# Performance work log

Measured on AMD Instinct MI355X. Metric: run time of the kernel, lower is better.

The kernel has to match this reference:

```python
import jax, jax.numpy as jnp
import numpy as np

NDIM = 3
IMG_SIZE = (192, 192, 192)
CPS = (5, 5, 5)
CP_GRID = (42, 42, 42)


def bspline_kernel_1d(stride):
    # cubic B-spline sampled at (i - radius)/stride, length 4*stride-1
    n = 4 * stride - 1
    t = np.abs((np.arange(n) - n // 2) / float(stride))
    vals = np.where(t < 1.0, 2.0 / 3.0 + (0.5 * t - 1.0) * t ** 2,
                    np.where(t < 2.0, -((t - 2.0) ** 3) / 6.0, 0.0))
    return jnp.asarray(vals, dtype=jnp.float32)


def conv_transpose1d_lastaxis(x, kernel, stride, padding):
    # depthwise transposed conv along last axis; same kernel for every channel,
    # so fold all leading dims into the batch and use a single-channel conv
    # with lhs_dilation (equivalent to conv_transpose; kernel is symmetric).
    shp = x.shape
    K = kernel.shape[0]
    x2 = x.reshape(-1, 1, shp[-1])  # [N, C=1, L]
    w = kernel.reshape(1, 1, K)     # [O, I, W]
    pad = K - 1 - padding
    y = jax.lax.conv_general_dilated(
        x2, w, window_strides=(1,), padding=[(pad, pad)],
        lhs_dilation=(stride,), dimension_numbers=("NCW", "OIW", "NCW"))
    return y.reshape(shp[:-1] + (y.shape[-1],))


def setup_inputs() -> dict:
    key = jax.random.key(0)
    v = jax.random.normal(key, (4, NDIM) + CP_GRID, dtype=jnp.float32)
    return {"v": v}


def reference(v) -> jnp.ndarray:
    kernels = [bspline_kernel_1d(s) for s in CPS]
    for i in range(NDIM):
        k = kernels[i]
        s = CPS[i]
        p = (k.shape[0] - 1) // 2
        x = jnp.moveaxis(v, i + 2, -1)
        x = conv_transpose1d_lastaxis(x, k, s, p)
        v = jnp.moveaxis(x, -1, i + 2)
    # crop: slice(s, s + img_size) per spatial dim
    slicer = (slice(None), slice(None)) + tuple(
        slice(CPS[i], CPS[i] + IMG_SIZE[i]) for i in range(NDIM))
    return v[slicer]
```

## Files before the change

### kernel.cpp

```cpp
#include <hip/hip_runtime.h>


#define CPN 42
#define IMG 192
#define TXX 6
#define TYY 6
#define NTHREADS 256
#define SLICE (CPN * CPN * CPN)

__device__ __forceinline__ float bsp_w_rt(int r, int d) {
  double f = (double)r / 5.0;
  double g = (double)(5 - r) / 5.0;
  double w;
  if (d == 0)      { w = g * g * g / 6.0; }
  else if (d == 1) { w = 2.0 / 3.0 + (0.5 * f - 1.0) * f * f; }
  else if (d == 2) { w = 2.0 / 3.0 + (0.5 * g - 1.0) * g * g; }
  else             { w = f * f * f / 6.0; }
  return (float)w;
}

__global__ void __launch_bounds__(NTHREADS) ffd_kernel(
    const float* __restrict__ v, float* __restrict__ out) {
  const int tid = threadIdx.x;
  const int w = tid >> 6;
  const int lane = tid & 63;
  const int bx = blockIdx.x;
  const int by = blockIdx.y;
  const int sl = blockIdx.z;
  const int x0 = bx * TXX;
  const int y0 = by * TYY;

  __shared__ float wtab[20];
  if (tid < 20) wtab[tid] = bsp_w_rt(tid >> 2, tid & 3);
  __syncthreads();

  const int q = lane < 48 ? lane : 47;
  const int c0 = (4 * q) / 5;
  float wz[4][5];
#pragma unroll
  for (int k = 0; k < 4; ++k) {
    int z = 4 * q + k;
    int c = z / 5;
    int r = z - 5 * c;
    int off = c - c0;
#pragma unroll
    for (int t = 0; t < 5; ++t) {
      int d = t - off;
      wz[k][t] = (d >= 0 && d < 4) ? wtab[r * 4 + d] : 0.0f;
    }
  }

  const float* vs = v + (size_t)sl * SLICE;
  float* os = out + (size_t)sl * ((size_t)IMG * IMG * IMG);
  const int cc = lane < 42 ? lane : 41;

  for (int i = 0; i < 9; ++i) {
    int col = w + 4 * i;
    int xi = col / 6;
    int yi = col - 6 * xi;
    int x = x0 + xi;
    int y = y0 + yi;
    int ax = x / 5, rx = x - 5 * ax;
    int ay = y / 5, ry = y - 5 * ay;
    float wx0 = wtab[rx * 4 + 0], wx1 = wtab[rx * 4 + 1];
    float wx2 = wtab[rx * 4 + 2], wx3 = wtab[rx * 4 + 3];
    float wy0 = wtab[ry * 4 + 0], wy1 = wtab[ry * 4 + 1];
    float wy2 = wtab[ry * 4 + 2], wy3 = wtab[ry * 4 + 3];

    const float* vb = vs + (ax * CPN + ay) * CPN + cc;
    float t2 = 0.0f;
#pragma unroll
    for (int dx = 0; dx < 4; ++dx) {
      const float* vp = vb + dx * (CPN * CPN);
      float s = wy0 * vp[0];
      s = fmaf(wy1, vp[CPN], s);
      s = fmaf(wy2, vp[2 * CPN], s);
      s = fmaf(wy3, vp[3 * CPN], s);
      float wx = (dx == 0) ? wx0 : (dx == 1) ? wx1 : (dx == 2) ? wx2 : wx3;
      t2 = fmaf(wx, s, t2);
    }

    int t2i = __float_as_int(t2);
    float s[5];
#pragma unroll
    for (int t = 0; t < 5; ++t)
      s[t] = __int_as_float(
          __builtin_amdgcn_ds_bpermute((c0 + t) << 2, t2i));

    float res[4];
#pragma unroll
    for (int k = 0; k < 4; ++k) {
      float a = wz[k][0] * s[0];
      a = fmaf(wz[k][1], s[1], a);
      a = fmaf(wz[k][2], s[2], a);
      a = fmaf(wz[k][3], s[3], a);
      a = fmaf(wz[k][4], s[4], a);
      res[k] = a;
    }

    if (lane < 48) {
      float4 val = make_float4(res[0], res[1], res[2], res[3]);
      *reinterpret_cast<float4*>(
          os + (size_t)(x * IMG + y) * IMG + 4 * lane) = val;
    }
  }
}

extern "C" void kernel_launch(void* const* d_in, const int* in_sizes, int n_in,
                              void* d_out, int out_size, void* d_ws, size_t ws_size,
                              hipStream_t stream) {
  (void)in_sizes; (void)n_in; (void)d_ws; (void)ws_size; (void)out_size;
  const float* v = (const float*)d_in[0];
  float* out = (float*)d_out;
  dim3 grid(IMG / TXX, IMG / TYY, 12);
  ffd_kernel<<<grid, NTHREADS, 0, stream>>>(v, out);
}
```

Before: 386.0 us.

## Restructure B-spline upsampling into per-x-plane separable passes through shared memory

Each block now handles one output x-plane of one slice. It first collapses the x-direction into a control-point plane in LDS, then expands along y into a second LDS buffer, and finally applies the z weights and writes full rows. This removes the redundant 16-point global gathers per output column and the cross-lane permutes. The block index is also swizzled across slices. The cost is extra LDS use and barriers, with some idle lanes in the z pass.

Result: faster. 349.8 us (-9.4%).

```diff
diff --git a/kernel.cpp b/kernel.cpp
--- a/kernel.cpp
+++ b/kernel.cpp
@@ -3,10 +3,12 @@
 
 #define CPN 42
 #define IMG 192
-#define TXX 6
-#define TYY 6
 #define NTHREADS 256
 #define SLICE (CPN * CPN * CPN)
+#define PLANE (CPN * CPN)
+#define NBLK (12 * IMG)
+
+typedef float v4f __attribute__((ext_vector_type(4)));
 
 __device__ __forceinline__ float bsp_w_rt(int r, int d) {
   double f = (double)r / 5.0;
@@ -22,20 +24,28 @@
 __global__ void __launch_bounds__(NTHREADS) ffd_kernel(
     const float* __restrict__ v, float* __restrict__ out) {
   const int tid = threadIdx.x;
-  const int w = tid >> 6;
+  const int bid = blockIdx.x;
+  const int n  = (bid & 7) * (NBLK / 8) + (bid >> 3);
+  const int sl = n / IMG;
+  const int x  = n - sl * IMG;
+  const int ax = x / 5;
+  const int rx = x - 5 * ax;
+
+  __shared__ v4f  wq[5];
+  __shared__ float t1[PLANE];
+  __shared__ float t2[IMG * CPN];
+
+  if (tid < 5) {
+    v4f qv;
+    qv.x = bsp_w_rt(tid, 0); qv.y = bsp_w_rt(tid, 1);
+    qv.z = bsp_w_rt(tid, 2); qv.w = bsp_w_rt(tid, 3);
+    wq[tid] = qv;
+  }
+
+  const int w    = tid >> 6;
   const int lane = tid & 63;
-  const int bx = blockIdx.x;
-  const int by = blockIdx.y;
-  const int sl = blockIdx.z;
-  const int x0 = bx * TXX;
-  const int y0 = by * TYY;
-
-  __shared__ float wtab[20];
-  if (tid < 20) wtab[tid] = bsp_w_rt(tid >> 2, tid & 3);
-  __syncthreads();
-
-  const int q = lane < 48 ? lane : 47;
-  const int c0 = (4 * q) / 5;
+  const int q    = lane < 48 ? lane : 47;
+  const int c0   = (4 * q) / 5;
   float wz[4][5];
 #pragma unroll
   for (int k = 0; k < 4; ++k) {
@@ -46,63 +56,54 @@
 #pragma unroll
     for (int t = 0; t < 5; ++t) {
       int d = t - off;
-      wz[k][t] = (d >= 0 && d < 4) ? wtab[r * 4 + d] : 0.0f;
+      wz[k][t] = (d >= 0 && d < 4) ? bsp_w_rt(r, d) : 0.0f;
     }
   }
+  __syncthreads();
 
-  const float* vs = v + (size_t)sl * SLICE;
-  float* os = out + (size_t)sl * ((size_t)IMG * IMG * IMG);
-  const int cc = lane < 42 ? lane : 41;
+  const float* vp0 = v + (size_t)sl * SLICE + (size_t)ax * PLANE;
+  const v4f wx = wq[rx];
+  for (int l = tid; l < PLANE; l += NTHREADS) {
+    float a = wx.x * vp0[l];
+    a = fmaf(wx.y, vp0[l + PLANE], a);
+    a = fmaf(wx.z, vp0[l + 2 * PLANE], a);
+    a = fmaf(wx.w, vp0[l + 3 * PLANE], a);
+    t1[l] = a;
+  }
+  __syncthreads();
 
-  for (int i = 0; i < 9; ++i) {
-    int col = w + 4 * i;
-    int xi = col / 6;
-    int yi = col - 6 * xi;
-    int x = x0 + xi;
-    int y = y0 + yi;
-    int ax = x / 5, rx = x - 5 * ax;
-    int ay = y / 5, ry = y - 5 * ay;
-    float wx0 = wtab[rx * 4 + 0], wx1 = wtab[rx * 4 + 1];
-    float wx2 = wtab[rx * 4 + 2], wx3 = wtab[rx * 4 + 3];
-    float wy0 = wtab[ry * 4 + 0], wy1 = wtab[ry * 4 + 1];
-    float wy2 = wtab[ry * 4 + 2], wy3 = wtab[ry * 4 + 3];
+  for (int l = tid; l < IMG * CPN; l += NTHREADS) {
+    int y  = l / CPN;
+    int cz = l - y * CPN;
+    int ay = y / 5;
+    int ry = y - 5 * ay;
+    v4f wy = wq[ry];
+    const float* tp = &t1[ay * CPN + cz];
+    float a = wy.x * tp[0];
+    a = fmaf(wy.y, tp[CPN], a);
+    a = fmaf(wy.z, tp[2 * CPN], a);
+    a = fmaf(wy.w, tp[3 * CPN], a);
+    t2[l] = a;
+  }
+  __syncthreads();
 
-    const float* vb = vs + (ax * CPN + ay) * CPN + cc;
-    float t2 = 0.0f;
-#pragma unroll
-    for (int dx = 0; dx < 4; ++dx) {
-      const float* vp = vb + dx * (CPN * CPN);
-      float s = wy0 * vp[0];
-      s = fmaf(wy1, vp[CPN], s);
-      s = fmaf(wy2, vp[2 * CPN], s);
-      s = fmaf(wy3, vp[3 * CPN], s);
-      float wx = (dx == 0) ? wx0 : (dx == 1) ? wx1 : (dx == 2) ? wx2 : wx3;
-      t2 = fmaf(wx, s, t2);
-    }
-
-    int t2i = __float_as_int(t2);
-    float s[5];
-#pragma unroll
-    for (int t = 0; t < 5; ++t)
-      s[t] = __int_as_float(
-          __builtin_amdgcn_ds_bpermute((c0 + t) << 2, t2i));
-
-    float res[4];
+  float* ob = out + (size_t)n * (IMG * IMG);
+  for (int i = 0; i < 48; ++i) {
+    int y = w + 4 * i;
+    const float* tp = &t2[y * CPN + c0];
+    float s0 = tp[0], s1 = tp[1], s2 = tp[2], s3 = tp[3], s4 = tp[4];
+    v4f res;
 #pragma unroll
     for (int k = 0; k < 4; ++k) {
-      float a = wz[k][0] * s[0];
-      a = fmaf(wz[k][1], s[1], a);
-      a = fmaf(wz[k][2], s[2], a);
-      a = fmaf(wz[k][3], s[3], a);
-      a = fmaf(wz[k][4], s[4], a);
+      float a = wz[k][0] * s0;
+      a = fmaf(wz[k][1], s1, a);
+      a = fmaf(wz[k][2], s2, a);
+      a = fmaf(wz[k][3], s3, a);
+      a = fmaf(wz[k][4], s4, a);
       res[k] = a;
     }
-
-    if (lane < 48) {
-      float4 val = make_float4(res[0], res[1], res[2], res[3]);
-      *reinterpret_cast<float4*>(
-          os + (size_t)(x * IMG + y) * IMG + 4 * lane) = val;
-    }
+    if (lane < 48)
+      *reinterpret_cast<v4f*>(ob + y * IMG + 4 * q) = res;
   }
 }
 
@@ -112,6 +113,5 @@
   (void)in_sizes; (void)n_in; (void)d_ws; (void)ws_size; (void)out_size;
   const float* v = (const float*)d_in[0];
   float* out = (float*)d_out;
-  dim3 grid(IMG / TXX, IMG / TYY, 12);
-  ffd_kernel<<<grid, NTHREADS, 0, stream>>>(v, out);
+  ffd_kernel<<<dim3(NBLK), NTHREADS, 0, stream>>>(v, out);
 }
```
